# Optimization experiments

Measured on AMD Instinct MI355X. Metric: run time of the kernel, lower is better.

The kernel has to match this reference:

```python
import jax, jax.numpy as jnp
import numpy as np

N_NODES = 100000
N_ANCHORS = 32
EMB_DIM = 64


def setup_inputs() -> dict:
    key = jax.random.key(0)
    k1, k2, k3, k4, k5 = jax.random.split(key, 5)
    embeds = jax.random.normal(k1, (N_NODES, EMB_DIM), dtype=jnp.float32)
    dists_array = jax.random.uniform(k2, (N_NODES, N_ANCHORS), dtype=jnp.float32)
    # torch Linear(2*D, D): y = x @ W.T + b; we store W already transposed [2D, D]
    W_hidden = jax.random.normal(k3, (2 * EMB_DIM, EMB_DIM), dtype=jnp.float32) * (1.0 / np.sqrt(2 * EMB_DIM))
    b_hidden = jax.random.normal(k4, (EMB_DIM,), dtype=jnp.float32) * 0.01
    anchorset_id = jax.random.randint(k5, (N_ANCHORS,), 0, N_NODES)
    return {
        "embeds": embeds,
        "dists_array": dists_array,
        "W_hidden": W_hidden,
        "b_hidden": b_hidden,
        "anchorset_id": anchorset_id,
    }


def reference(embeds, dists_array, W_hidden, b_hidden, anchorset_id):
    # embeds: [N, D]; dists_array: [N, A]; anchorset_id: [A]
    set_emb = embeds[anchorset_id]                         # gather -> [A, D]
    msg_anchor = dists_array[:, :, None] * set_emb[None]   # [N, A, D]
    self_feat = jnp.broadcast_to(embeds[:, None, :], msg_anchor.shape)  # [N, A, D]
    messages = jnp.concatenate((msg_anchor, self_feat), axis=-1)        # [N, A, 2D]
    hidden = jnp.einsum('nae,ed->nad', messages, W_hidden) + b_hidden   # [N, A, D]
    return hidden.mean(axis=1)                              # [N, D]
```

## Files before the change

kernel.cpp:

```cpp
#include <hip/hip_runtime.h>
#include <cstdint>
#include <cstddef>


#define N_NODES 100000
#define DIM     64
#define NTILES  1563
#define GRID    768
#define AS_K    104

typedef short bf16x8 __attribute__((ext_vector_type(8)));
typedef float f32x4  __attribute__((ext_vector_type(4)));

__device__ __forceinline__ unsigned short f2bf(float f) {
    union { float f; unsigned u; } c; c.f = f;
    return (unsigned short)((c.u + 0x7fffu + ((c.u >> 16) & 1u)) >> 16);
}
__device__ __forceinline__ float bf2f(unsigned short h) {
    union { unsigned u; float f; } c; c.u = ((unsigned)h) << 16; return c.f;
}
__device__ __forceinline__ unsigned long long pack4h(float a, float b, float c, float d) {
    unsigned short h0 = f2bf(a), h1 = f2bf(b), h2 = f2bf(c), h3 = f2bf(d);
    return (unsigned long long)h0 | ((unsigned long long)h1 << 16) |
           ((unsigned long long)h2 << 32) | ((unsigned long long)h3 << 48);
}
__device__ __forceinline__ unsigned long long pack4l(float a, float b, float c, float d) {
    unsigned short l0 = f2bf(a - bf2f(f2bf(a))), l1 = f2bf(b - bf2f(f2bf(b)));
    unsigned short l2 = f2bf(c - bf2f(f2bf(c))), l3 = f2bf(d - bf2f(f2bf(d)));
    return (unsigned long long)l0 | ((unsigned long long)l1 << 16) |
           ((unsigned long long)l2 << 32) | ((unsigned long long)l3 << 48);
}

__global__ __launch_bounds__(256) void pnn_prep(
    const float* __restrict__ embeds, const float* __restrict__ W,
    const int* __restrict__ aid, unsigned short* __restrict__ fragB)
{
    const int b = blockIdx.x, tid = threadIdx.x;
    if (b < 8) {
        const int t = b * 256 + tid;
        const int a = t >> 6, d = t & 63;
        const float* se = embeds + (size_t)aid[a] * DIM;
        float s = 0.f;
        #pragma unroll
        for (int e = 0; e < DIM; ++e) s += se[e] * W[e * DIM + d];
        s *= (1.0f / 32.0f);
        const int j = a & 7, quad = a >> 3;
        const int nt = d >> 4, col = d & 15;
        const int lane = quad * 16 + col;
        const unsigned short hi = f2bf(s);
        fragB[((nt * 2 + 0) * 64 + lane) * 8 + j] = hi;
        fragB[((nt * 2 + 1) * 64 + lane) * 8 + j] = f2bf(s - bf2f(hi));
    } else {
        const int w = (b - 8) * 256 + tid;
        const int j    = w & 7;
        const int lane = (w >> 3) & 63;
        const int pl   = (w >> 9) & 1;
        const int nt   = (w >> 10) & 3;
        const int ks   = 1 + (w >> 12);
        const int k = ks * 32 + (lane >> 4) * 8 + j;
        const int n = nt * 16 + (lane & 15);
        const float v = W[(k + 32) * DIM + n];
        unsigned short h = f2bf(v);
        if (pl) h = f2bf(v - bf2f(h));
        fragB[(((ks * 4 + nt) * 2 + pl) * 64 + lane) * 8 + j] = h;
    }
}

#define LOAD_TILE(m0)                                                          \
    do {                                                                       \
        const float4* dg = (const float4*)(dists + (size_t)(m0) * 32);         \
        _Pragma("unroll")                                                      \
        for (int i = 0; i < 2; ++i) {                                          \
            const int f = i * 256 + tid;                                       \
            dv[i] = ((m0) + (f >> 3) < N_NODES) ? dg[f]                        \
                                                : make_float4(0.f,0.f,0.f,0.f);\
        }                                                                      \
        const float4* eg = (const float4*)(embeds + (size_t)(m0) * 64);        \
        _Pragma("unroll")                                                      \
        for (int i = 0; i < 4; ++i) {                                          \
            const int f = i * 256 + tid;                                       \
            ev[i] = ((m0) + (f >> 4) < N_NODES) ? eg[f]                        \
                                                : make_float4(0.f,0.f,0.f,0.f);\
        }                                                                      \
    } while (0)

__global__ __launch_bounds__(256, 3) void pnn_main(
    const float* __restrict__ embeds,
    const float* __restrict__ dists,
    const unsigned short* __restrict__ fragB,
    const float* __restrict__ bias,
    float* __restrict__ out)
{
    __shared__ __align__(16) unsigned short sB[12288];
    __shared__ __align__(16) unsigned short As[2][4][16][AS_K];

    const int tid  = threadIdx.x;
    const int wave = tid >> 6;
    const int lane = tid & 63;
    const int quad = lane >> 4;
    const int col  = lane & 15;

    #pragma unroll
    for (int i = 0; i < 6; ++i)
        ((uint4*)sB)[i * 256 + tid] = ((const uint4*)fragB)[i * 256 + tid];

    float bias_n[4];
    #pragma unroll
    for (int nt = 0; nt < 4; ++nt) bias_n[nt] = bias[nt * 16 + col];

    int tile = blockIdx.x;
    float4 dv[2], ev[4];
    LOAD_TILE(tile * 64);

    for (; tile < NTILES; tile += GRID) {
        const int n0 = tile * 64;

        #pragma unroll
        for (int i = 0; i < 2; ++i) {
            const int f  = i * 256 + tid;
            const int nd = f >> 3, k0 = (f & 7) * 4;
            const float4 v = dv[i];
            *(unsigned long long*)&As[0][nd >> 4][nd & 15][k0] = pack4h(v.x, v.y, v.z, v.w);
            *(unsigned long long*)&As[1][nd >> 4][nd & 15][k0] = pack4l(v.x, v.y, v.z, v.w);
        }
        #pragma unroll
        for (int i = 0; i < 4; ++i) {
            const int f  = i * 256 + tid;
            const int nd = f >> 4, k0 = 32 + (f & 15) * 4;
            const float4 v = ev[i];
            *(unsigned long long*)&As[0][nd >> 4][nd & 15][k0] = pack4h(v.x, v.y, v.z, v.w);
            *(unsigned long long*)&As[1][nd >> 4][nd & 15][k0] = pack4l(v.x, v.y, v.z, v.w);
        }
        __syncthreads();

        const int t2 = tile + GRID;
        if (t2 < NTILES) {
            LOAD_TILE(t2 * 64);
        }

        f32x4 acc[4];
        #pragma unroll
        for (int nt = 0; nt < 4; ++nt) {
            const float bb = bias_n[nt];
            acc[nt][0] = bb; acc[nt][1] = bb; acc[nt][2] = bb; acc[nt][3] = bb;
        }
        const bf16x8* Bl = (const bf16x8*)sB;
        #pragma unroll
        for (int ks = 0; ks < 3; ++ks) {
            const bf16x8 Ahi = *(const bf16x8*)&As[0][wave][col][ks * 32 + quad * 8];
            const bf16x8 Alo = *(const bf16x8*)&As[1][wave][col][ks * 32 + quad * 8];
            #pragma unroll
            for (int nt = 0; nt < 4; ++nt) {
                const bf16x8 Bh = Bl[((ks * 4 + nt) * 2 + 0) * 64 + lane];
                const bf16x8 Bo = Bl[((ks * 4 + nt) * 2 + 1) * 64 + lane];
                acc[nt] = __builtin_amdgcn_mfma_f32_16x16x32_bf16(Ahi, Bh, acc[nt], 0, 0, 0);
                acc[nt] = __builtin_amdgcn_mfma_f32_16x16x32_bf16(Ahi, Bo, acc[nt], 0, 0, 0);
                acc[nt] = __builtin_amdgcn_mfma_f32_16x16x32_bf16(Alo, Bh, acc[nt], 0, 0, 0);
            }
        }

        #pragma unroll
        for (int r = 0; r < 4; ++r) {
            const int node = n0 + wave * 16 + quad * 4 + r;
            if (node < N_NODES) {
                float* po = out + (size_t)node * DIM + col;
                #pragma unroll
                for (int nt = 0; nt < 4; ++nt) po[nt * 16] = acc[nt][r];
            }
        }
        __syncthreads();
    }
}

extern "C" void kernel_launch(void* const* d_in, const int* in_sizes, int n_in,
                              void* d_out, int out_size, void* d_ws, size_t ws_size,
                              hipStream_t stream) {
    const float* embeds = (const float*)d_in[0];
    const float* dists  = (const float*)d_in[1];
    const float* W      = (const float*)d_in[2];
    const float* bias   = (const float*)d_in[3];
    const int*   aid    = (const int*)d_in[4];
    float* out = (float*)d_out;

    unsigned short* fragB = (unsigned short*)d_ws;

    pnn_prep<<<40, 256, 0, stream>>>(embeds, W, aid, fragB);
    pnn_main<<<GRID, 256, 0, stream>>>(embeds, dists, fragB, bias, out);
}
```

Measured before the change: 94.14 us.

## Fuse weight prep into main kernel, computing anchor projection per block via MFMA

Removes the separate prep kernel and its workspace round-trip. Each block now converts the self-feature half of W into split-bf16 fragments directly in shared memory, and computes the anchor-embedding projection (set_emb @ W_top, scaled by 1/32) with MFMAs on two waves. This saves a kernel launch and the serialization between the two kernels. In exchange, all 768 blocks redundantly do the prep work and read W from global memory before starting their tiles.

Result: no change. 94.42 us (+0.3%).

```diff
diff --git a/kernel.cpp b/kernel.cpp
--- a/kernel.cpp
+++ b/kernel.cpp
@@ -29,41 +29,6 @@
     unsigned short l2 = f2bf(c - bf2f(f2bf(c))), l3 = f2bf(d - bf2f(f2bf(d)));
     return (unsigned long long)l0 | ((unsigned long long)l1 << 16) |
            ((unsigned long long)l2 << 32) | ((unsigned long long)l3 << 48);
-}
-
-__global__ __launch_bounds__(256) void pnn_prep(
-    const float* __restrict__ embeds, const float* __restrict__ W,
-    const int* __restrict__ aid, unsigned short* __restrict__ fragB)
-{
-    const int b = blockIdx.x, tid = threadIdx.x;
-    if (b < 8) {
-        const int t = b * 256 + tid;
-        const int a = t >> 6, d = t & 63;
-        const float* se = embeds + (size_t)aid[a] * DIM;
-        float s = 0.f;
-        #pragma unroll
-        for (int e = 0; e < DIM; ++e) s += se[e] * W[e * DIM + d];
-        s *= (1.0f / 32.0f);
-        const int j = a & 7, quad = a >> 3;
-        const int nt = d >> 4, col = d & 15;
-        const int lane = quad * 16 + col;
-        const unsigned short hi = f2bf(s);
-        fragB[((nt * 2 + 0) * 64 + lane) * 8 + j] = hi;
-        fragB[((nt * 2 + 1) * 64 + lane) * 8 + j] = f2bf(s - bf2f(hi));
-    } else {
-        const int w = (b - 8) * 256 + tid;
-        const int j    = w & 7;
-        const int lane = (w >> 3) & 63;
-        const int pl   = (w >> 9) & 1;
-        const int nt   = (w >> 10) & 3;
-        const int ks   = 1 + (w >> 12);
-        const int k = ks * 32 + (lane >> 4) * 8 + j;
-        const int n = nt * 16 + (lane & 15);
-        const float v = W[(k + 32) * DIM + n];
-        unsigned short h = f2bf(v);
-        if (pl) h = f2bf(v - bf2f(h));
-        fragB[(((ks * 4 + nt) * 2 + pl) * 64 + lane) * 8 + j] = h;
-    }
 }
 
 #define LOAD_TILE(m0)                                                          \
@@ -84,11 +49,12 @@
         }                                                                      \
     } while (0)
 
-__global__ __launch_bounds__(256, 3) void pnn_main(
+__global__ __launch_bounds__(256, 3) void pnn_fused(
     const float* __restrict__ embeds,
     const float* __restrict__ dists,
-    const unsigned short* __restrict__ fragB,
+    const float* __restrict__ W,
     const float* __restrict__ bias,
+    const int*   __restrict__ aid,
     float* __restrict__ out)
 {
     __shared__ __align__(16) unsigned short sB[12288];
@@ -100,17 +66,84 @@
     const int quad = lane >> 4;
     const int col  = lane & 15;
 
+    int tile = blockIdx.x;
+    float4 dv[2], ev[4];
+    LOAD_TILE(tile * 64);
+
     #pragma unroll
-    for (int i = 0; i < 6; ++i)
-        ((uint4*)sB)[i * 256 + tid] = ((const uint4*)fragB)[i * 256 + tid];
+    for (int i = 0; i < 16; ++i) {
+        const int e  = i * 256 + tid;
+        const int n  = e & 63;
+        const int kk = e >> 6;
+        const float v = W[(kk + 64) * DIM + n];
+        const int ks  = 1 + (kk >> 5);
+        const int rem = kk & 31;
+        const int jj  = rem & 7;
+        const int ln2 = (rem >> 3) * 16 + (n & 15);
+        const int nt  = n >> 4;
+        const unsigned short hi = f2bf(v);
+        sB[(((ks * 4 + nt) * 2 + 0) * 64 + ln2) * 8 + jj] = hi;
+        sB[(((ks * 4 + nt) * 2 + 1) * 64 + ln2) * 8 + jj] = f2bf(v - bf2f(hi));
+    }
+
+    #pragma unroll
+    for (int i = 0; i < 2; ++i) {
+        const int fa  = i * 256 + tid;
+        const int row = fa >> 4;
+        const int c4  = fa & 15;
+        const float4 v = ((const float4*)(embeds + (size_t)aid[row] * DIM))[c4];
+        *(unsigned long long*)&As[0][row >> 4][row & 15][c4 * 4] = pack4h(v.x, v.y, v.z, v.w);
+        *(unsigned long long*)&As[1][row >> 4][row & 15][c4 * 4] = pack4l(v.x, v.y, v.z, v.w);
+    }
+    __syncthreads();
+
+    if (wave < 2) {
+        f32x4 accP[4];
+        #pragma unroll
+        for (int nt = 0; nt < 4; ++nt) accP[nt] = (f32x4){0.f, 0.f, 0.f, 0.f};
+        #pragma unroll
+        for (int ks2 = 0; ks2 < 2; ++ks2) {
+            const bf16x8 Ahi = *(const bf16x8*)&As[0][wave][col][ks2 * 32 + quad * 8];
+            const bf16x8 Alo = *(const bf16x8*)&As[1][wave][col][ks2 * 32 + quad * 8];
+            #pragma unroll
+            for (int nt = 0; nt < 4; ++nt) {
+                float w8[8];
+                #pragma unroll
+                for (int j = 0; j < 8; ++j)
+                    w8[j] = W[(ks2 * 32 + quad * 8 + j) * DIM + nt * 16 + col];
+                bf16x8 Bh, Bo;
+                #pragma unroll
+                for (int j = 0; j < 8; ++j) {
+                    const unsigned short h = f2bf(w8[j]);
+                    Bh[j] = (short)h;
+                    Bo[j] = (short)f2bf(w8[j] - bf2f(h));
+                }
+                accP[nt] = __builtin_amdgcn_mfma_f32_16x16x32_bf16(Ahi, Bh, accP[nt], 0, 0, 0);
+                accP[nt] = __builtin_amdgcn_mfma_f32_16x16x32_bf16(Alo, Bh, accP[nt], 0, 0, 0);
+                accP[nt] = __builtin_amdgcn_mfma_f32_16x16x32_bf16(Ahi, Bo, accP[nt], 0, 0, 0);
+            }
+        }
+        #pragma unroll
+        for (int r = 0; r < 4; ++r) {
+            const int a  = wave * 16 + quad * 4 + r;
+            const int jj = a & 7;
+            const int q2 = a >> 3;
+            #pragma unroll
+            for (int nt = 0; nt < 4; ++nt) {
+                const float s = accP[nt][r] * (1.0f / 32.0f);
+                const int ln2 = q2 * 16 + col;
+                const unsigned short hi = f2bf(s);
+                sB[((nt * 2 + 0) * 64 + ln2) * 8 + jj] = hi;
+                sB[((nt * 2 + 1) * 64 + ln2) * 8 + jj] = f2bf(s - bf2f(hi));
+            }
+        }
+    }
 
     float bias_n[4];
     #pragma unroll
     for (int nt = 0; nt < 4; ++nt) bias_n[nt] = bias[nt * 16 + col];
 
-    int tile = blockIdx.x;
-    float4 dv[2], ev[4];
-    LOAD_TILE(tile * 64);
+    __syncthreads();
 
     for (; tile < NTILES; tile += GRID) {
         const int n0 = tile * 64;
@@ -181,9 +214,7 @@
     const float* bias   = (const float*)d_in[3];
     const int*   aid    = (const int*)d_in[4];
     float* out = (float*)d_out;
-
-    unsigned short* fragB = (unsigned short*)d_ws;
-
-    pnn_prep<<<40, 256, 0, stream>>>(embeds, W, aid, fragB);
-    pnn_main<<<GRID, 256, 0, stream>>>(embeds, dists, fragB, bias, out);
-}
+    (void)d_ws; (void)ws_size;
+
+    pnn_fused<<<GRID, 256, 0, stream>>>(embeds, dists, W, bias, aid, out);
+}
```
